# Optimization experiments

Hardware: AMD Instinct MI355X
Metric: run time of the kernel (lower is better)

The kernel has to match this reference:

```python
import jax, jax.numpy as jnp
import numpy as np

NUM_HEADS = 16
ROPE_BASE = 10000.0
MAX_POS = 4096


def _rope_tables(head_dim):
    inv_freq = 1.0 / (ROPE_BASE ** (np.arange(0, head_dim, 2, dtype=np.float32) / head_dim))
    freqs = np.arange(MAX_POS, dtype=np.float32)[:, None] * inv_freq[None, :]
    emb = np.concatenate([freqs, freqs], axis=-1)  # [MAX_POS, head_dim]
    return jnp.asarray(np.cos(emb)), jnp.asarray(np.sin(emb))


def _rotate_half(x):
    d = x.shape[-1] // 2
    return jnp.concatenate([-x[..., d:], x[..., :d]], axis=-1)


def _apply_rope(x, pos, cos_t, sin_t):
    # x: [B,H,S,D], pos: [B,S]
    cos = cos_t[pos][:, None]  # [B,1,S,D]
    sin = sin_t[pos][:, None]
    return x * cos + _rotate_half(x) * sin


def setup_inputs() -> dict:
    key = jax.random.key(0)
    ks = jax.random.split(key, 8)
    B, N, M, C = 2, 2048, 2048, 1024
    s = 1.0 / np.sqrt(C)
    return {
        "query": jax.random.normal(ks[0], (B, N, C), jnp.float32),
        "key": jax.random.normal(ks[1], (B, M, C), jnp.float32),
        "query_pos": jnp.broadcast_to(jnp.arange(N, dtype=jnp.int32), (B, N)),
        "key_pos": jnp.broadcast_to(jnp.arange(M, dtype=jnp.int32), (B, M)),
        "Wq": jax.random.normal(ks[2], (C, C), jnp.float32) * s,
        "bq": jnp.zeros((C,), jnp.float32),
        "Wk": jax.random.normal(ks[3], (C, C), jnp.float32) * s,
        "Wv": jax.random.normal(ks[4], (C, C), jnp.float32) * s,
        "bv": jnp.zeros((C,), jnp.float32),
        "Wo": jax.random.normal(ks[5], (C, C), jnp.float32) * s,
        "bo": jnp.zeros((C,), jnp.float32),
    }


def reference(query, key, query_pos, key_pos, Wq, bq, Wk, Wv, bv, Wo, bo):
    B, N, C = query.shape
    M = key.shape[1]
    H = NUM_HEADS
    D = C // H
    scale = D ** -0.5
    cos_t, sin_t = _rope_tables(D)

    value = key  # value defaults to key
    identity = query

    q = (query @ Wq.T + bq).reshape(B, N, H, D).transpose(0, 2, 1, 3)
    k = (key @ Wk.T).reshape(B, M, H, D).transpose(0, 2, 1, 3)
    v = (value @ Wv.T + bv).reshape(B, M, H, D).transpose(0, 2, 1, 3)

    q = _apply_rope(q, query_pos, cos_t, sin_t)
    k = _apply_rope(k, key_pos, cos_t, sin_t)

    attn = jnp.einsum('bhnd,bhmd->bhnm', q, k) * scale
    attn = jax.nn.softmax(attn, axis=-1)
    x = jnp.einsum('bhnm,bhmd->bhnd', attn, v)  # [B,H,N,D]
    x = x.transpose(0, 2, 1, 3).reshape(B, N, C)
    x = x @ Wo.T + bo
    return x + identity
```

## Files before the change

kernel.cpp:

```cpp
#include <hip/hip_runtime.h>
#include <hip/hip_bf16.h>
#include <stdint.h>

#define B_ 2
#define N_ 2048
#define M_ 2048
#define C_ 1024
#define H_ 16
#define D_ 64

typedef __attribute__((ext_vector_type(8))) short s16x8;
typedef __attribute__((ext_vector_type(4))) short s16x4;
typedef __attribute__((ext_vector_type(4))) float f32x4;
typedef __attribute__((ext_vector_type(16))) float f32x16;

__device__ __attribute__((always_inline)) inline short f2b(float f){
    __hip_bfloat16 h = __float2bfloat16(f); short s; __builtin_memcpy(&s, &h, 2); return s;
}
__device__ __attribute__((always_inline)) inline float b2f(short s){
    __hip_bfloat16 h; __builtin_memcpy(&h, &s, 2); return __bfloat162float(h);
}

#define MFMA16(a,b,c) __builtin_amdgcn_mfma_f32_16x16x32_bf16(a,b,c,0,0,0)
#define MFMA32(a,b,c) __builtin_amdgcn_mfma_f32_32x32x16_bf16(a,b,c,0,0,0)

__device__ __attribute__((always_inline)) inline void gl_lds16(const void* g, void* l){
    __builtin_amdgcn_global_load_lds((__attribute__((address_space(1))) void*)g,
                                     (__attribute__((address_space(3))) void*)l, 16, 0, 0);
}
__device__ __attribute__((always_inline)) inline unsigned fbits(float f){
    unsigned u; __builtin_memcpy(&u, &f, 4); return u;
}
__device__ __attribute__((always_inline)) inline unsigned cvtpk(float lo, float hi){
    unsigned r;
    asm("v_cvt_pk_bf16_f32 %0, %1, %2" : "=v"(r) : "v"(lo), "v"(hi));
    return r;
}
__device__ __attribute__((always_inline)) inline void lane32swap(unsigned &a, unsigned &b){
    asm("v_permlane32_swap_b32 %0, %1" : "+v"(a), "+v"(b));
}

__global__ void cvt_all(const float* __restrict__ q, const float* __restrict__ k,
                        const float* __restrict__ wq, const float* __restrict__ wk,
                        const float* __restrict__ wv, const float* __restrict__ wo,
                        short* __restrict__ dst){
    long i = ((long)blockIdx.x * 256 + threadIdx.x) * 8;
    const float* src; long off;
    if      (i <  4194304L){ src = q;  off = i; }
    else if (i <  8388608L){ src = k;  off = i - 4194304L; }
    else if (i <  9437184L){ src = wq; off = i - 8388608L; }
    else if (i < 10485760L){ src = wk; off = i - 9437184L; }
    else if (i < 11534336L){ src = wv; off = i - 10485760L; }
    else                   { src = wo; off = i - 11534336L; }
    float4 a = *(const float4*)(src + off);
    float4 b = *(const float4*)(src + off + 4);
    s16x8 o;
    o[0]=f2b(a.x); o[1]=f2b(a.y); o[2]=f2b(a.z); o[3]=f2b(a.w);
    o[4]=f2b(b.x); o[5]=f2b(b.y); o[6]=f2b(b.z); o[7]=f2b(b.w);
    *(s16x8*)(dst + i) = o;
}

__global__ __launch_bounds__(256, 3) void gemm_qkv(
    const short* __restrict__ qbf, const short* __restrict__ kbf,
    const short* __restrict__ W,
    const float* __restrict__ bq, const float* __restrict__ bv,
    short* __restrict__ qproj, short* __restrict__ kproj, short* __restrict__ vT)
{
    __shared__ short As[128 * 32];
    __shared__ short Bs[128 * 32];
    const int n0 = blockIdx.x * 128, m0 = blockIdx.y * 128;
    const int sel = n0 >> 10;
    const short* A = (sel == 0) ? qbf : kbf;
    const int tid = threadIdx.x, lane = tid & 63, wave = tid >> 6;
    const int quad = lane >> 4, l16 = lane & 15;
    const int wr = (wave >> 1) * 64, wc = (wave & 1) * 64;
    const int srow = lane >> 2, scol = (lane & 3) * 8;

    f32x4 acc[4][4] = {};

    const short* Ag = A + (size_t)(m0 + wave * 32 + srow) * C_ + scol;
    const short* Bg = W + (size_t)(n0 + wave * 32 + srow) * C_ + scol;
    short* lA0 = As + (wave * 32) * 32;
    short* lA1 = As + (wave * 32 + 16) * 32;
    short* lB0 = Bs + (wave * 32) * 32;
    short* lB1 = Bs + (wave * 32 + 16) * 32;

    for (int k0 = 0; k0 < C_; k0 += 32){
        __syncthreads();
        gl_lds16(Ag + k0, lA0);
        gl_lds16(Ag + k0 + 16 * (size_t)C_, lA1);
        gl_lds16(Bg + k0, lB0);
        gl_lds16(Bg + k0 + 16 * (size_t)C_, lB1);
        __syncthreads();
        s16x8 af[4], bfr[4];
        #pragma unroll
        for (int t = 0; t < 4; t++) af[t]  = *(const s16x8*)&As[(wr + t*16 + l16) * 32 + quad * 8];
        #pragma unroll
        for (int t = 0; t < 4; t++) bfr[t] = *(const s16x8*)&Bs[(wc + t*16 + l16) * 32 + quad * 8];
        #pragma unroll
        for (int i = 0; i < 4; i++)
            #pragma unroll
            for (int j = 0; j < 4; j++)
                acc[i][j] = MFMA16(af[i], bfr[j], acc[i][j]);
    }

    if (sel <= 1){
        short* dst = sel ? kproj : qproj;
        const float* bp = sel ? nullptr : bq;
        const int coff = sel << 10;
        #pragma unroll
        for (int j = 0; j < 4; j++){
            int c = n0 + wc + j * 16 + l16 - coff;
            float bb = bp ? bp[c] : 0.0f;
            #pragma unroll
            for (int i = 0; i < 4; i++){
                int row = m0 + wr + i * 16 + quad * 4;
                #pragma unroll
                for (int r = 0; r < 4; r++)
                    dst[(size_t)(row + r) * C_ + c] = f2b(acc[i][j][r] + bb);
            }
        }
    } else {
        #pragma unroll
        for (int j = 0; j < 4; j++){
            int col = n0 - 2048 + wc + j * 16 + l16;
            int h = col >> 6, d = col & 63;
            float bb = bv[col];
            #pragma unroll
            for (int i = 0; i < 4; i++){
                int row = m0 + wr + i * 16 + quad * 4;
                int b = row >> 11, m = row & 2047;
                unsigned u0 = (unsigned)(unsigned short)f2b(acc[i][j][0] + bb) |
                              ((unsigned)(unsigned short)f2b(acc[i][j][1] + bb) << 16);
                unsigned u1 = (unsigned)(unsigned short)f2b(acc[i][j][2] + bb) |
                              ((unsigned)(unsigned short)f2b(acc[i][j][3] + bb) << 16);
                uint2 u; u.x = u0; u.y = u1;
                *(uint2*)&vT[(((size_t)(b * H_ + h)) * D_ + d) * M_ + m] = u;
            }
        }
    }
}

__global__ __launch_bounds__(256, 4) void gemm_out(
    const short* __restrict__ A, const short* __restrict__ W,
    const float* __restrict__ bias, const float* __restrict__ resid,
    float* __restrict__ outf)
{
    __shared__ short As[128 * 32];
    __shared__ short Bs[64 * 32];
    const int n0 = blockIdx.x * 64, m0 = blockIdx.y * 128;
    const int tid = threadIdx.x, lane = tid & 63, wave = tid >> 6;
    const int quad = lane >> 4, l16 = lane & 15;
    const int srow = lane >> 2, scol = (lane & 3) * 8;

    f32x4 acc[2][4] = {};
    const short* Ag = A + (size_t)(m0 + wave * 32 + srow) * C_ + scol;
    const short* Bg = W + (size_t)(n0 + wave * 16 + srow) * C_ + scol;
    short* lA0 = As + (wave * 32) * 32;
    short* lA1 = As + (wave * 32 + 16) * 32;
    short* lB  = Bs + (wave * 16) * 32;

    for (int k0 = 0; k0 < C_; k0 += 32){
        __syncthreads();
        gl_lds16(Ag + k0, lA0);
        gl_lds16(Ag + k0 + 16 * (size_t)C_, lA1);
        gl_lds16(Bg + k0, lB);
        __syncthreads();
        s16x8 af[2], bfr[4];
        #pragma unroll
        for (int t = 0; t < 2; t++) af[t]  = *(const s16x8*)&As[(wave*32 + t*16 + l16) * 32 + quad * 8];
        #pragma unroll
        for (int t = 0; t < 4; t++) bfr[t] = *(const s16x8*)&Bs[(t*16 + l16) * 32 + quad * 8];
        #pragma unroll
        for (int i = 0; i < 2; i++)
            #pragma unroll
            for (int j = 0; j < 4; j++)
                acc[i][j] = MFMA16(af[i], bfr[j], acc[i][j]);
    }

    #pragma unroll
    for (int j = 0; j < 4; j++){
        int c = n0 + j * 16 + l16;
        float bb = bias[c];
        #pragma unroll
        for (int i = 0; i < 2; i++){
            int row = m0 + wave * 32 + i * 16 + quad * 4;
            #pragma unroll
            for (int r = 0; r < 4; r++){
                size_t idx = (size_t)(row + r) * C_ + c;
                outf[idx] = acc[i][j][r] + bb + resid[idx];
            }
        }
    }
}

__global__ void rope_k(short* __restrict__ k, const int* __restrict__ kpos){
    int t = blockIdx.x * blockDim.x + threadIdx.x;
    int i = t & 31;
    int h = (t >> 5) & (H_ - 1);
    int row = t >> 9;
    int pos = kpos[row];
    short* base = k + (size_t)row * C_ + h * D_;
    float x1 = b2f(base[i]), x2 = b2f(base[i + 32]);
    float invf = exp2f((float)i * (-13.287712379549449f / 32.0f));
    float f = (float)pos * invf;
    float c = __cosf(f), s = __sinf(f);
    base[i]      = f2b(x1 * c - x2 * s);
    base[i + 32] = f2b(x2 * c + x1 * s);
}

__global__ __launch_bounds__(256, 4) void flash_attn(
    const short* __restrict__ q, const short* __restrict__ k,
    const short* __restrict__ vt, short* __restrict__ o,
    const int* __restrict__ qpos)
{
    __shared__ short smem[17920];
    const int b = blockIdx.y >> 4, h = blockIdx.y & 15;
    const int n0 = blockIdx.x * 64;
    const int tid = threadIdx.x, lane = tid & 63, wave = tid >> 6;
    const int hi = lane >> 5, l32 = lane & 31;
    const int wq = wave & 1, kq = wave >> 1;

    s16x8 qf[4];
    const float fac = 0.18033688011112042f;
    {
        int qrow = n0 + wq * 32 + l32;
        const short* qg = &q[((size_t)(b * N_ + qrow)) * C_ + h * D_];
        float pos = (float)qpos[b * N_ + qrow];
        s16x8 raw[4];
        #pragma unroll
        for (int c = 0; c < 4; c++) raw[c] = *(const s16x8*)&qg[c * 16 + hi * 8];
        #pragma unroll
        for (int c = 0; c < 2; c++){
            s16x8 olo, ohi8;
            #pragma unroll
            for (int j = 0; j < 8; j++){
                int irot = c * 16 + hi * 8 + j;
                float invf = exp2f((float)irot * (-13.287712379549449f / 32.0f));
                float ang = pos * invf;
                float cs = __cosf(ang), sn = __sinf(ang);
                float x1 = b2f(raw[c][j]), x2 = b2f(raw[c + 2][j]);
                olo[j]  = f2b((x1 * cs - x2 * sn) * fac);
                ohi8[j] = f2b((x2 * cs + x1 * sn) * fac);
            }
            qf[c] = olo; qf[c + 2] = ohi8;
        }
    }

    const short* kg = k  + (size_t)(b * M_) * C_ + h * D_;
    const short* vg = vt + ((size_t)(b * H_ + h)) * D_ * M_;
    const int srow0 = tid >> 3, sseg = (tid & 7) * 8;

    union V8 { s16x8 v; uint2 u[2]; };
    V8 kreg[2], vreg[2];

    #pragma unroll
    for (int ii = 0; ii < 2; ii++){
        int row = srow0 + 32 * ii;
        kreg[ii].v = *(const s16x8*)&kg[(size_t)row * C_ + sseg];
        vreg[ii].v = *(const s16x8*)&vg[(size_t)row * M_ + sseg];
    }
    #pragma unroll
    for (int ii = 0; ii < 2; ii++){
        int row = srow0 + 32 * ii;
        short* kd = &smem[row * 68 + sseg];
        *(uint2*)kd = kreg[ii].u[0]; *(uint2*)(kd + 4) = kreg[ii].u[1];
        short* vd = &smem[8704 + row * 68 + sseg];
        *(uint2*)vd = vreg[ii].u[0]; *(uint2*)(vd + 4) = vreg[ii].u[1];
    }

    f32x16 zero16 = {};
    f32x16 oacc[2] = {zero16, zero16};
    float lacc = 0.f;

    for (int st = 0; st < 32; st++){
        const int p = st & 1;
        __syncthreads();
        if (st < 31){
            #pragma unroll
            for (int ii = 0; ii < 2; ii++){
                int row = srow0 + 32 * ii;
                kreg[ii].v = *(const s16x8*)&kg[((size_t)((st + 1) * 64 + row)) * C_ + sseg];
                vreg[ii].v = *(const s16x8*)&vg[(size_t)row * M_ + (st + 1) * 64 + sseg];
            }
        }
        const short* Kp = &smem[p * 4352];
        const short* Vp = &smem[8704 + p * 4352];

        s16x4 kf[4][2];
        #pragma unroll
        for (int c = 0; c < 4; c++){
            const short* a = &Kp[(kq * 32 + l32) * 68 + c * 16 + hi * 8];
            kf[c][0] = *(const s16x4*)a; kf[c][1] = *(const s16x4*)(a + 4);
        }
        s16x8 vf[2][2];
        #pragma unroll
        for (int dt = 0; dt < 2; dt++)
            #pragma unroll
            for (int c = 0; c < 2; c++){
                const short* a = &Vp[(dt * 32 + l32) * 68 + kq * 32 + c * 16 + hi * 8];
                vf[dt][c] = __builtin_shufflevector(*(const s16x4*)a, *(const s16x4*)(a + 4),
                                                    0,1,2,3,4,5,6,7);
            }

        f32x16 sv = {};
        #pragma unroll
        for (int c = 0; c < 4; c++){
            s16x8 ka = __builtin_shufflevector(kf[c][0], kf[c][1], 0,1,2,3,4,5,6,7);
            sv = MFMA32(ka, qf[c], sv);
        }
        float pe[16];
        #pragma unroll
        for (int e = 0; e < 16; e++) pe[e] = __builtin_amdgcn_exp2f(sv[e]);
        float ls = 0.f;
        #pragma unroll
        for (int e = 0; e < 16; e += 4) ls += (pe[e] + pe[e+1]) + (pe[e+2] + pe[e+3]);
        lacc += ls;
        s16x8 pf[2];
        #pragma unroll
        for (int c = 0; c < 2; c++){
            unsigned a1 = cvtpk(pe[8*c + 0], pe[8*c + 1]);
            unsigned a2 = cvtpk(pe[8*c + 2], pe[8*c + 3]);
            unsigned b1 = cvtpk(pe[8*c + 4], pe[8*c + 5]);
            unsigned b2 = cvtpk(pe[8*c + 6], pe[8*c + 7]);
            lane32swap(a1, b1);
            lane32swap(a2, b2);
            union { unsigned u[4]; s16x8 v; } pk;
            pk.u[0] = a1; pk.u[1] = a2; pk.u[2] = b1; pk.u[3] = b2;
            pf[c] = pk.v;
        }

        #pragma unroll
        for (int dt = 0; dt < 2; dt++)
            #pragma unroll
            for (int c = 0; c < 2; c++)
                oacc[dt] = MFMA32(pf[c], vf[dt][c], oacc[dt]);

        if (st < 31){
            int pn = p ^ 1;
            #pragma unroll
            for (int ii = 0; ii < 2; ii++){
                int row = srow0 + 32 * ii;
                short* kd = &smem[pn * 4352 + row * 68 + sseg];
                *(uint2*)kd = kreg[ii].u[0]; *(uint2*)(kd + 4) = kreg[ii].u[1];
                short* vd = &smem[8704 + pn * 4352 + row * 68 + sseg];
                *(uint2*)vd = vreg[ii].u[0]; *(uint2*)(vd + 4) = vreg[ii].u[1];
            }
        }
    }

    __syncthreads();

    float* LO   = (float*)smem;
    float* Lsum = (float*)&smem[17408];
    float* Linv = Lsum + 64;

    float l0 = lacc + __shfl_xor(lacc, 32);

    if (kq == 1){
        Lsum[wq * 32 + l32] = l0;
        #pragma unroll
        for (int dt = 0; dt < 2; dt++)
            #pragma unroll
            for (int e = 0; e < 16; e++){
                int qrow = wq * 32 + (e & 3) + 8 * (e >> 2) + 4 * hi;
                LO[qrow * 65 + dt * 32 + l32] = oacc[dt][e];
            }
    }
    __syncthreads();
    if (kq == 0){
        float lt = l0 + Lsum[wq * 32 + l32];
        Linv[wq * 32 + l32] = 1.0f / lt;
        asm volatile("s_waitcnt lgkmcnt(0)" ::: "memory");
        #pragma unroll
        for (int dt = 0; dt < 2; dt++)
            #pragma unroll
            for (int e = 0; e < 16; e++){
                int qrow = wq * 32 + (e & 3) + 8 * (e >> 2) + 4 * hi;
                float val = (oacc[dt][e] + LO[qrow * 65 + dt * 32 + l32]) * Linv[qrow];
                o[((size_t)(b * N_ + n0 + qrow)) * C_ + h * D_ + dt * 32 + l32] = f2b(val);
            }
    }
}

extern "C" void kernel_launch(void* const* d_in, const int* in_sizes, int n_in,
                              void* d_out, int out_size, void* d_ws, size_t ws_size,
                              hipStream_t stream) {
    const float* query = (const float*)d_in[0];
    const float* key   = (const float*)d_in[1];
    const int*   qpos  = (const int*)d_in[2];
    const int*   kpos  = (const int*)d_in[3];
    const float* Wq    = (const float*)d_in[4];
    const float* bq    = (const float*)d_in[5];
    const float* Wk    = (const float*)d_in[6];
    const float* Wv    = (const float*)d_in[7];
    const float* bv    = (const float*)d_in[8];
    const float* Wo    = (const float*)d_in[9];
    const float* bo    = (const float*)d_in[10];
    float* out = (float*)d_out;

    const size_t E4M = (size_t)4 * 1024 * 1024;
    const size_t E1M = (size_t)1024 * 1024;
    short* ws    = (short*)d_ws;
    short* qbf   = ws;
    short* kbf   = qbf   + E4M;
    short* wqkvb = kbf   + E4M;
    short* wob   = wqkvb + 3 * E1M;
    short* qproj = wob   + E1M;
    short* kproj = qproj + E4M;
    short* vT    = kproj + E4M;
    short* attn  = qbf;

    cvt_all<<<6144, 256, 0, stream>>>(query, key, Wq, Wk, Wv, Wo, ws);

    gemm_qkv<<<dim3(24, 32), 256, 0, stream>>>(qbf, kbf, wqkvb, bq, bv,
                                               qproj, kproj, vT);

    rope_k<<<(B_ * M_ * H_ * 32) / 256, 256, 0, stream>>>(kproj, kpos);

    flash_attn<<<dim3(32, 32), 256, 0, stream>>>(qproj, kproj, vT, attn, qpos);

    gemm_out<<<dim3(16, 32), 256, 0, stream>>>(attn, wob, bo, query, out);
}
```

Baseline: 220.9 us.

## Fuse key RoPE into QKV GEMM epilogue and widen flash-attention blocks

Rotary embedding for the keys now runs inside the QKV projection GEMM epilogue, using fp32 accumulators, which removes the separate rope_k kernel and its read-modify-write pass over kproj. The flash-attention kernel now uses 512 threads and 128 query rows per block, so each K/V tile staged in shared memory serves twice as many queries and each thread loads one row instead of two. The reduction buffers are resized to fit. The trade-off is that launch_bounds(512,4) asks for twice as many resident waves per CU, which squeezes registers and could cause spills. Halving the grid also reduces the number of blocks available to spread across the GPU.

```diff
diff --git a/kernel.cpp b/kernel.cpp
--- a/kernel.cpp
+++ b/kernel.cpp
@@ -64,6 +64,7 @@
     const short* __restrict__ qbf, const short* __restrict__ kbf,
     const short* __restrict__ W,
     const float* __restrict__ bq, const float* __restrict__ bv,
+    const int* __restrict__ kpos,
     short* __restrict__ qproj, short* __restrict__ kproj, short* __restrict__ vT)
 {
     __shared__ short As[128 * 32];
@@ -104,20 +105,37 @@
                 acc[i][j] = MFMA16(af[i], bfr[j], acc[i][j]);
     }
 
-    if (sel <= 1){
-        short* dst = sel ? kproj : qproj;
-        const float* bp = sel ? nullptr : bq;
-        const int coff = sel << 10;
+    if (sel == 0){
         #pragma unroll
         for (int j = 0; j < 4; j++){
-            int c = n0 + wc + j * 16 + l16 - coff;
-            float bb = bp ? bp[c] : 0.0f;
+            int c = n0 + wc + j * 16 + l16;
+            float bb = bq[c];
             #pragma unroll
             for (int i = 0; i < 4; i++){
                 int row = m0 + wr + i * 16 + quad * 4;
                 #pragma unroll
                 for (int r = 0; r < 4; r++)
-                    dst[(size_t)(row + r) * C_ + c] = f2b(acc[i][j][r] + bb);
+                    qproj[(size_t)(row + r) * C_ + c] = f2b(acc[i][j][r] + bb);
+            }
+        }
+    } else if (sel == 1){
+        #pragma unroll
+        for (int j2 = 0; j2 < 2; j2++){
+            int c1 = n0 - 1024 + wc + j2 * 16 + l16;
+            int irot = c1 & 63;
+            float invf = exp2f((float)irot * (-13.287712379549449f / 32.0f));
+            #pragma unroll
+            for (int i = 0; i < 4; i++){
+                int row = m0 + wr + i * 16 + quad * 4;
+                #pragma unroll
+                for (int r = 0; r < 4; r++){
+                    float pos = (float)kpos[row + r];
+                    float ang = pos * invf;
+                    float cs = __cosf(ang), sn = __sinf(ang);
+                    float x1 = acc[i][j2][r], x2 = acc[i][j2 + 2][r];
+                    kproj[(size_t)(row + r) * C_ + c1]      = f2b(x1 * cs - x2 * sn);
+                    kproj[(size_t)(row + r) * C_ + c1 + 32] = f2b(x2 * cs + x1 * sn);
+                }
             }
         }
     } else {
@@ -194,32 +212,17 @@
     }
 }
 
-__global__ void rope_k(short* __restrict__ k, const int* __restrict__ kpos){
-    int t = blockIdx.x * blockDim.x + threadIdx.x;
-    int i = t & 31;
-    int h = (t >> 5) & (H_ - 1);
-    int row = t >> 9;
-    int pos = kpos[row];
-    short* base = k + (size_t)row * C_ + h * D_;
-    float x1 = b2f(base[i]), x2 = b2f(base[i + 32]);
-    float invf = exp2f((float)i * (-13.287712379549449f / 32.0f));
-    float f = (float)pos * invf;
-    float c = __cosf(f), s = __sinf(f);
-    base[i]      = f2b(x1 * c - x2 * s);
-    base[i + 32] = f2b(x2 * c + x1 * s);
-}
-
-__global__ __launch_bounds__(256, 4) void flash_attn(
+__global__ __launch_bounds__(512, 4) void flash_attn(
     const short* __restrict__ q, const short* __restrict__ k,
     const short* __restrict__ vt, short* __restrict__ o,
     const int* __restrict__ qpos)
 {
     __shared__ short smem[17920];
     const int b = blockIdx.y >> 4, h = blockIdx.y & 15;
-    const int n0 = blockIdx.x * 64;
+    const int n0 = blockIdx.x * 128;
     const int tid = threadIdx.x, lane = tid & 63, wave = tid >> 6;
     const int hi = lane >> 5, l32 = lane & 31;
-    const int wq = wave & 1, kq = wave >> 1;
+    const int wq = wave & 3, kq = wave >> 2;
 
     s16x8 qf[4];
     const float fac = 0.18033688011112042f;
@@ -252,21 +255,15 @@
     const int srow0 = tid >> 3, sseg = (tid & 7) * 8;
 
     union V8 { s16x8 v; uint2 u[2]; };
-    V8 kreg[2], vreg[2];
-
-    #pragma unroll
-    for (int ii = 0; ii < 2; ii++){
-        int row = srow0 + 32 * ii;
-        kreg[ii].v = *(const s16x8*)&kg[(size_t)row * C_ + sseg];
-        vreg[ii].v = *(const s16x8*)&vg[(size_t)row * M_ + sseg];
-    }
-    #pragma unroll
-    for (int ii = 0; ii < 2; ii++){
-        int row = srow0 + 32 * ii;
-        short* kd = &smem[row * 68 + sseg];
-        *(uint2*)kd = kreg[ii].u[0]; *(uint2*)(kd + 4) = kreg[ii].u[1];
-        short* vd = &smem[8704 + row * 68 + sseg];
-        *(uint2*)vd = vreg[ii].u[0]; *(uint2*)(vd + 4) = vreg[ii].u[1];
+    V8 kreg, vreg;
+
+    kreg.v = *(const s16x8*)&kg[(size_t)srow0 * C_ + sseg];
+    vreg.v = *(const s16x8*)&vg[(size_t)srow0 * M_ + sseg];
+    {
+        short* kd = &smem[srow0 * 68 + sseg];
+        *(uint2*)kd = kreg.u[0]; *(uint2*)(kd + 4) = kreg.u[1];
+        short* vd = &smem[8704 + srow0 * 68 + sseg];
+        *(uint2*)vd = vreg.u[0]; *(uint2*)(vd + 4) = vreg.u[1];
     }
 
     f32x16 zero16 = {};
@@ -277,12 +274,8 @@
         const int p = st & 1;
         __syncthreads();
         if (st < 31){
-            #pragma unroll
-            for (int ii = 0; ii < 2; ii++){
-                int row = srow0 + 32 * ii;
-                kreg[ii].v = *(const s16x8*)&kg[((size_t)((st + 1) * 64 + row)) * C_ + sseg];
-                vreg[ii].v = *(const s16x8*)&vg[(size_t)row * M_ + (st + 1) * 64 + sseg];
-            }
+            kreg.v = *(const s16x8*)&kg[((size_t)((st + 1) * 64 + srow0)) * C_ + sseg];
+            vreg.v = *(const s16x8*)&vg[(size_t)srow0 * M_ + (st + 1) * 64 + sseg];
         }
         const short* Kp = &smem[p * 4352];
         const short* Vp = &smem[8704 + p * 4352];
@@ -338,14 +331,10 @@
 
         if (st < 31){
             int pn = p ^ 1;
-            #pragma unroll
-            for (int ii = 0; ii < 2; ii++){
-                int row = srow0 + 32 * ii;
-                short* kd = &smem[pn * 4352 + row * 68 + sseg];
-                *(uint2*)kd = kreg[ii].u[0]; *(uint2*)(kd + 4) = kreg[ii].u[1];
-                short* vd = &smem[8704 + pn * 4352 + row * 68 + sseg];
-                *(uint2*)vd = vreg[ii].u[0]; *(uint2*)(vd + 4) = vreg[ii].u[1];
-            }
+            short* kd = &smem[pn * 4352 + srow0 * 68 + sseg];
+            *(uint2*)kd = kreg.u[0]; *(uint2*)(kd + 4) = kreg.u[1];
+            short* vd = &smem[8704 + pn * 4352 + srow0 * 68 + sseg];
+            *(uint2*)vd = vreg.u[0]; *(uint2*)(vd + 4) = vreg.u[1];
         }
     }
 
@@ -353,7 +342,7 @@
 
     float* LO   = (float*)smem;
     float* Lsum = (float*)&smem[17408];
-    float* Linv = Lsum + 64;
+    float* Linv = Lsum + 128;
 
     float l0 = lacc + __shfl_xor(lacc, 32);
 
@@ -413,12 +402,10 @@
 
     cvt_all<<<6144, 256, 0, stream>>>(query, key, Wq, Wk, Wv, Wo, ws);
 
-    gemm_qkv<<<dim3(24, 32), 256, 0, stream>>>(qbf, kbf, wqkvb, bq, bv,
+    gemm_qkv<<<dim3(24, 32), 256, 0, stream>>>(qbf, kbf, wqkvb, bq, bv, kpos,
                                                qproj, kproj, vT);
 
-    rope_k<<<(B_ * M_ * H_ * 32) / 256, 256, 0, stream>>>(kproj, kpos);
-
-    flash_attn<<<dim3(32, 32), 256, 0, stream>>>(qproj, kproj, vT, attn, qpos);
+    flash_attn<<<dim3(16, 32), 512, 0, stream>>>(qproj, kproj, vT, attn, qpos);
 
     gemm_out<<<dim3(16, 32), 256, 0, stream>>>(attn, wob, bo, query, out);
 }
```

Result: faster. 206.9 us (-6.4%).
